# Optimization experiments

Hardware: AMD Instinct MI355X
Metric: run time of the kernel (lower is better)

Reference implementation:

```python
import jax, jax.numpy as jnp
import numpy as np

N = 100000   # nodes
E = 1000000  # edges (before self-loops)
F = 64       # feat_dim
H = 64       # hidden_dim
G = 512      # graphs in batch
EPS = 1e-5   # BatchNorm1d eps


def setup_inputs() -> dict:
    key = jax.random.key(0)
    ks = jax.random.split(key, 16)
    inp = {}
    inp["x"] = jax.random.normal(ks[0], (N, F), dtype=jnp.float32)
    inp["edge_index"] = jax.random.randint(ks[1], (2, E), 0, N)
    inp["batch"] = jnp.sort(jax.random.randint(ks[2], (N,), 0, G))
    dims = [(F, H), (H, H), (H, H)]
    for i, (di, do) in enumerate(dims):
        # xavier_uniform-scale weights, zero bias (as in weights_init)
        bound = np.sqrt(6.0 / (di + do)).astype(np.float32)
        inp[f"W{i}"] = jax.random.uniform(ks[3 + i], (do, di), dtype=jnp.float32,
                                          minval=-bound, maxval=bound)
        inp[f"b{i}"] = jnp.zeros((do,), dtype=jnp.float32)
        inp[f"g{i}"] = jnp.ones((do,), dtype=jnp.float32)
        inp[f"beta{i}"] = jnp.zeros((do,), dtype=jnp.float32)
    return inp


def reference(x, edge_index, batch,
              W0, b0, g0, beta0,
              W1, b1, g1, beta1,
              W2, b2, g2, beta2):
    # PyG GCNConv: add self-loops, norm = deg^-1/2[src] * deg^-1/2[dst]
    loops = jnp.arange(N)
    src = jnp.concatenate([edge_index[0], loops])  # source j
    dst = jnp.concatenate([edge_index[1], loops])  # target i
    deg = jax.ops.segment_sum(jnp.ones(src.shape, x.dtype), dst, num_segments=N)
    dinv = jnp.where(deg > 0, jax.lax.rsqrt(deg), 0.0)
    norm = dinv[src] * dinv[dst]  # [E+N]

    params = [(W0, b0, g0, beta0), (W1, b1, g1, beta1), (W2, b2, g2, beta2)]
    xs = []
    h = x
    for (W, b, g, beta) in params:
        h = h @ W.T                               # lin (no bias)
        msg = h[src] * norm[:, None]              # gather + scale  [E+N, H]
        h = jax.ops.segment_sum(msg, dst, num_segments=N) + b  # scatter-add + bias
        h = jax.nn.relu(h)
        # BatchNorm1d (training mode: biased batch stats)
        mean = h.mean(axis=0)
        var = h.var(axis=0)
        h = g * (h - mean) * jax.lax.rsqrt(var + EPS) + beta
        xs.append(h)

    # global_add_pool per layer output, then concat
    pooled = [jax.ops.segment_sum(xi, batch, num_segments=G) for xi in xs]
    global_rep = jnp.concatenate(pooled, axis=1)  # [G, 3*H]
    return global_rep, h
```

## Files before the change

### kernel.cpp

```cpp
#include <hip/hip_runtime.h>

#define HD 64
#define BN_EPS 1e-5f

typedef unsigned int u32;
typedef __attribute__((ext_vector_type(8))) short bfrag;
typedef __attribute__((ext_vector_type(4))) float ffrag;

__device__ __forceinline__ unsigned tobf(float x) {
    unsigned u = __float_as_uint(x);
    return (u + 0x7fffu + ((u >> 16) & 1u)) >> 16;
}
__device__ __forceinline__ float bf_lo(unsigned u) { return __uint_as_float(u << 16); }
__device__ __forceinline__ float bf_hi(unsigned u) { return __uint_as_float(u & 0xffff0000u); }


__global__ void k_deg(const int* __restrict__ dst, int* __restrict__ deg,
                      int* __restrict__ rank, int E) {
    int e = blockIdx.x * blockDim.x + threadIdx.x;
    if (e < E) {
        int d = __builtin_nontemporal_load(&dst[e]);
        int r = atomicAdd(&deg[d], 1);
        __builtin_nontemporal_store(r, &rank[e]);
    }
}

__global__ void k_scan1(const int* __restrict__ deg, int* __restrict__ incl,
                        int* __restrict__ bsums, float* __restrict__ dinv,
                        unsigned* __restrict__ hWs, int N) {
    __shared__ int s[256];
    int tid = threadIdx.x;
    int i = blockIdx.x * 256 + tid;
    if (blockIdx.x == 0 && tid < 32) hWs[(size_t)N * 32 + tid] = 0u;
    int d = (i < N) ? deg[i] : 0;
    int pd = (i < N) ? ((d + 8) & ~7) : 0;
    s[tid] = pd;
    __syncthreads();
    for (int off = 1; off < 256; off <<= 1) {
        int t = (tid >= off) ? s[tid - off] : 0;
        __syncthreads();
        s[tid] += t;
        __syncthreads();
    }
    if (i < N) {
        incl[i] = s[tid];
        dinv[i] = rsqrtf((float)(d + 1));
    }
    if (tid == 255) bsums[blockIdx.x] = s[255];
}

__global__ void k_scan3(int* __restrict__ rowp, const int* __restrict__ deg,
                        const int* __restrict__ incl, const int* __restrict__ bsums,
                        int* __restrict__ ed, int N, int nb) {
    __shared__ float red[256];
    int tid = threadIdx.x;
    int b = blockIdx.x;
    float psum = 0.f;
    for (int t = tid; t < b; t += 256) psum += (float)bsums[t];
    red[tid] = psum;
    __syncthreads();
    for (int off = 128; off > 0; off >>= 1) {
        if (tid < off) red[tid] += red[tid + off];
        __syncthreads();
    }
    int bpre = (int)red[0];
    int i = b * 256 + tid;
    if (i < N) {
        int d = deg[i];
        int pd = (d + 8) & ~7;
        int rv = incl[i] - pd + bpre;
        rowp[i] = rv;
        ed[rv] = i;
        for (int k = d + 1; k < pd; k++) ed[rv + k] = N;
        if (i == N - 1) rowp[N] = rv + pd;
    }
}

#define FILL_SLAB 4096
__global__ void k_fill(const int* __restrict__ src, const int* __restrict__ dst,
                       const int* __restrict__ rank, const int* __restrict__ rowp,
                       int* __restrict__ ed, const int* __restrict__ batch,
                       int* __restrict__ cnt, int E, int N, int G) {
    int tid = threadIdx.x;
    int gid = blockIdx.x * 256 + tid;
    if (gid < G) {
        int g = gid;
        int lo = 0, hi = N;
        while (lo < hi) { int mid = (lo + hi) >> 1; if (batch[mid] < g) lo = mid + 1; else hi = mid; }
        int lo2 = lo, hi2 = N;
        while (lo2 < hi2) { int mid = (lo2 + hi2) >> 1; if (batch[mid] < g + 1) lo2 = mid + 1; else hi2 = mid; }
        cnt[g] = lo2 - lo;
    }
    int part = blockIdx.x & 7;
    int base = (blockIdx.x >> 3) * FILL_SLAB;
    int end = min(base + FILL_SLAB, E);
    for (int e = base + tid; e < end; e += 256) {
        int d = __builtin_nontemporal_load(&dst[e]);
        if (((d >> 12) & 7) == part) {
            int s = __builtin_nontemporal_load(&src[e]);
            int r = __builtin_nontemporal_load(&rank[e]);
            ed[rowp[d] + 1 + r] = s;
        }
    }
}

template<int FP32IN>
__global__ __launch_bounds__(256) void k_gemm2(const void* __restrict__ Aptr,
                                               const void* __restrict__ Wptr,
                                               const float* __restrict__ cb,
                                               const float* __restrict__ dinv,
                                               unsigned short* __restrict__ hWs,
                                               int N, int ntiles) {
    int lane = threadIdx.x & 63;
    int m = lane & 15, quad = lane >> 4;
    bfrag wf[4][2];
    if (FP32IN) {
        const float* W = (const float*)Wptr;
#pragma unroll
        for (int ft = 0; ft < 4; ft++)
#pragma unroll
            for (int kf = 0; kf < 2; kf++) {
                const float4* p4 = (const float4*)(W + (ft * 16 + m) * HD + kf * 32 + quad * 8);
                float4 x0 = p4[0], x1 = p4[1];
                union { unsigned u[4]; bfrag b; } r;
                r.u[0] = tobf(x0.x) | (tobf(x0.y) << 16);
                r.u[1] = tobf(x0.z) | (tobf(x0.w) << 16);
                r.u[2] = tobf(x1.x) | (tobf(x1.y) << 16);
                r.u[3] = tobf(x1.z) | (tobf(x1.w) << 16);
                wf[ft][kf] = r.b;
            }
    } else {
        const unsigned short* W = (const unsigned short*)Wptr;
#pragma unroll
        for (int ft = 0; ft < 4; ft++)
#pragma unroll
            for (int kf = 0; kf < 2; kf++)
                wf[ft][kf] = *(const bfrag*)(W + (ft * 16 + m) * HD + kf * 32 + quad * 8);
    }
    float cbv[4];
#pragma unroll
    for (int ft = 0; ft < 4; ft++) cbv[ft] = cb ? cb[ft * 16 + m] : 0.f;

    int wid = (blockIdx.x * blockDim.x + threadIdx.x) >> 6;
    int nw = (gridDim.x * blockDim.x) >> 6;
    for (int tile = wid; tile < ntiles; tile += nw) {
        int arow = min(tile * 16 + m, N - 1);
        bfrag a0, a1;
        if (FP32IN) {
            const float4* p4 = (const float4*)((const float*)Aptr + (size_t)arow * HD + quad * 8);
            float4 x0 = p4[0], x1 = p4[1], y0 = p4[8], y1 = p4[9];
            union { unsigned u[4]; bfrag b; } r0, r1;
            r0.u[0] = tobf(x0.x) | (tobf(x0.y) << 16);
            r0.u[1] = tobf(x0.z) | (tobf(x0.w) << 16);
            r0.u[2] = tobf(x1.x) | (tobf(x1.y) << 16);
            r0.u[3] = tobf(x1.z) | (tobf(x1.w) << 16);
            r1.u[0] = tobf(y0.x) | (tobf(y0.y) << 16);
            r1.u[1] = tobf(y0.z) | (tobf(y0.w) << 16);
            r1.u[2] = tobf(y1.x) | (tobf(y1.y) << 16);
            r1.u[3] = tobf(y1.z) | (tobf(y1.w) << 16);
            a0 = r0.b; a1 = r1.b;
        } else {
            const unsigned short* p = (const unsigned short*)Aptr + (size_t)arow * HD + quad * 8;
            a0 = *(const bfrag*)p;
            a1 = *(const bfrag*)(p + 32);
        }
        ffrag acc[4];
#pragma unroll
        for (int ft = 0; ft < 4; ft++) {
            acc[ft] = (ffrag){0.f, 0.f, 0.f, 0.f};
            acc[ft] = __builtin_amdgcn_mfma_f32_16x16x32_bf16(a0, wf[ft][0], acc[ft], 0, 0, 0);
            acc[ft] = __builtin_amdgcn_mfma_f32_16x16x32_bf16(a1, wf[ft][1], acc[ft], 0, 0, 0);
        }
        int r0n = tile * 16 + quad * 4;
        float dv[4];
#pragma unroll
        for (int r = 0; r < 4; r++) dv[r] = dinv[min(r0n + r, N - 1)];
#pragma unroll
        for (int ft = 0; ft < 4; ft++)
#pragma unroll
            for (int r = 0; r < 4; r++) {
                int nrow = r0n + r;
                if (nrow < N) {
                    float v = (acc[ft][r] + cbv[ft]) * dv[r];
                    hWs[(size_t)nrow * HD + ft * 16 + m] = (unsigned short)tobf(v);
                }
            }
    }
}

__global__ __launch_bounds__(256) void k_agg(const int* __restrict__ rowp,
                                             const int* __restrict__ ed,
                                             const float* __restrict__ dinv,
                                             const unsigned* __restrict__ hWs,
                                             const float* __restrict__ bias,
                                             const int* __restrict__ batch,
                                             void* __restrict__ outp, int outBf,
                                             float* __restrict__ stats,
                                             float* __restrict__ praw,
                                             int N, int chunk,
                                             const float* __restrict__ gam,
                                             const float* __restrict__ bet,
                                             float* __restrict__ ss,
                                             const float* __restrict__ Wnext,
                                             unsigned* __restrict__ Wfb,
                                             float* __restrict__ cf,
                                             float invN, int* __restrict__ ticket) {
    __shared__ u32 sbuf[4][2][1024];
    int tid = threadIdx.x;
    int lane = tid & 63;
    int hf = lane >> 5;
    int m = lane & 31;
    int lsel = lane >> 3;
    int fsel = lane & 7;
    int wv = tid >> 6;
    int wid = blockIdx.x * 4 + wv;
    int i0 = wid * chunk, i1 = min(i0 + chunk, N);
    const uint4* hW4 = (const uint4*)hWs;
    float b0 = bias[2 * m], b1 = bias[2 * m + 1];
    float bs0 = 0.f, bs1 = 0.f, bq0 = 0.f, bq1 = 0.f;
    int curb = -1;
    float p0 = 0.f, p1 = 0.f;
    if (i0 < N) {
        int idx = i0 + lane;
        int rowv = rowp[min(idx, N)];
        float dinvv = dinv[min(idx, N - 1)];
        int batchv = batch[min(idx, N - 1)];
        int s0g = __shfl(rowv, 0);
        int send = __shfl(rowv, i1 - i0);
        int i = i0, ln = 0;
        int rem = (__shfl(rowv, 1) - s0g) >> 3;
        float acc0 = 0.f, acc1 = 0.f;
        int nst = (send - s0g + 31) >> 5;
        int sb = s0g;
        int eidx;
        { int id = sb + m; eidx = (id < send) ? __builtin_nontemporal_load(&ed[id]) : N; }
#pragma unroll
        for (int j = 0; j < 4; j++) {
            int sj = __shfl(eidx, j * 8 + lsel);
            __builtin_amdgcn_global_load_lds(
                (const __attribute__((address_space(1))) u32*)(hW4 + (size_t)sj * 8 + fsel),
                (__attribute__((address_space(3))) u32*)(&sbuf[wv][0][j * 256]),
                16, 0, 0);
        }
        int eidxN = N;
        if (nst > 1) { int id = sb + 32 + m; eidxN = (id < send) ? __builtin_nontemporal_load(&ed[id]) : N; }
        for (int t = 0; t < nst; t++) {
            int cb = t & 1;
            asm volatile("s_waitcnt vmcnt(0)" ::: "memory");
            __builtin_amdgcn_sched_barrier(0);
            if (t + 1 < nst) {
#pragma unroll
                for (int j = 0; j < 4; j++) {
                    int sj = __shfl(eidxN, j * 8 + lsel);
                    __builtin_amdgcn_global_load_lds(
                        (const __attribute__((address_space(1))) u32*)(hW4 + (size_t)sj * 8 + fsel),
                        (__attribute__((address_space(3))) u32*)(&sbuf[wv][cb ^ 1][j * 256]),
                        16, 0, 0);
                }
                if (t + 2 < nst) { int id = sb + 64 + m; eidxN = (id < send) ? __builtin_nontemporal_load(&ed[id]) : N; }
            }
            const u32* cur = &sbuf[wv][cb][0];
            int ng = min(4, (send - sb) >> 3);
            for (int g = 0; g < ng; g++) {
                u32 u[4];
#pragma unroll
                for (int tt = 0; tt < 4; tt++)
                    u[tt] = cur[(g * 8 + hf + 2 * tt) * 32 + m];
#pragma unroll
                for (int tt = 0; tt < 4; tt++) { acc0 += bf_lo(u[tt]); acc1 += bf_hi(u[tt]); }
                if (--rem == 0) {
                    float s0 = acc0 + __shfl_xor(acc0, 32);
                    float s1 = acc1 + __shfl_xor(acc1, 32);
                    float di = __shfl(dinvv, ln);
                    int b = __shfl(batchv, ln);
                    float h0 = fmaxf(fmaf(di, s0, b0), 0.f);
                    float h1 = fmaxf(fmaf(di, s1, b1), 0.f);
                    if (lane < 32) {
                        if (outBf) ((unsigned*)outp)[(size_t)i * 32 + m] = tobf(h0) | (tobf(h1) << 16);
                        else ((float2*)outp)[(size_t)i * 32 + m] = make_float2(h0, h1);
                        bs0 += h0; bs1 += h1;
                        bq0 = fmaf(h0, h0, bq0); bq1 = fmaf(h1, h1, bq1);
                        if (b != curb) {
                            if (curb >= 0) {
                                atomicAdd(&praw[(size_t)curb * HD + 2 * m], p0);
                                atomicAdd(&praw[(size_t)curb * HD + 2 * m + 1], p1);
                            }
                            curb = b; p0 = h0; p1 = h1;
                        } else { p0 += h0; p1 += h1; }
                    }
                    i++; ln++;
                    rem = (i < i1) ? ((__shfl(rowv, ln + 1) - __shfl(rowv, ln)) >> 3)
                                   : 0x3fffffff;
                    acc0 = 0.f; acc1 = 0.f;
                }
            }
            sb += 32;
        }
    }
    if (lane < 32 && curb >= 0) {
        atomicAdd(&praw[(size_t)curb * HD + 2 * m], p0);
        atomicAdd(&praw[(size_t)curb * HD + 2 * m + 1], p1);
    }
    __shared__ float r1s[4][HD], r2s[4][HD];
    if (lane < 32) {
        r1s[wv][2 * m] = bs0; r1s[wv][2 * m + 1] = bs1;
        r2s[wv][2 * m] = bq0; r2s[wv][2 * m + 1] = bq1;
    }
    __syncthreads();
    if (tid < HD) {
        atomicAdd(&stats[tid], r1s[0][tid] + r1s[1][tid] + r1s[2][tid] + r1s[3][tid]);
        atomicAdd(&stats[HD + tid], r2s[0][tid] + r2s[1][tid] + r2s[2][tid] + r2s[3][tid]);
    }
    __shared__ int lastFlag;
    __syncthreads();
    if (tid == 0) {
        __threadfence();
        lastFlag = (atomicAdd(ticket, 1) == (int)gridDim.x - 1) ? 1 : 0;
    }
    __syncthreads();
    if (lastFlag) {
        __shared__ float lss[128];
        __shared__ float cpart[HD][4];
        if (tid < HD) {
            float s1v = atomicAdd(&stats[tid], 0.f);
            float s2v = atomicAdd(&stats[HD + tid], 0.f);
            float mean = s1v * invN;
            float var = s2v * invN - mean * mean;
            float sc = gam[tid] * rsqrtf(var + BN_EPS);
            float sh = bet[tid] - mean * sc;
            ss[tid] = sc; ss[64 + tid] = sh;
            lss[tid] = sc; lss[64 + tid] = sh;
        }
        __syncthreads();
        if (Wnext) {
            int r = tid >> 2, qs = (tid & 3) * 8;
            const float4* W4 = (const float4*)(Wnext + r * HD + 2 * qs);
            float c = 0.f;
#pragma unroll
            for (int t = 0; t < 4; t++) {
                float4 w = W4[t];
                int q = qs + 2 * t;
                Wfb[r * 32 + q]     = tobf(w.x * lss[2 * q])     | (tobf(w.y * lss[2 * q + 1]) << 16);
                Wfb[r * 32 + q + 1] = tobf(w.z * lss[2 * q + 2]) | (tobf(w.w * lss[2 * q + 3]) << 16);
                c = fmaf(lss[64 + 2 * q], w.x, c);
                c = fmaf(lss[64 + 2 * q + 1], w.y, c);
                c = fmaf(lss[64 + 2 * q + 2], w.z, c);
                c = fmaf(lss[64 + 2 * q + 3], w.w, c);
            }
            cpart[r][tid & 3] = c;
            __syncthreads();
            if (tid < HD)
                cf[tid] = cpart[tid][0] + cpart[tid][1] + cpart[tid][2] + cpart[tid][3];
        }
    }
}

__global__ __launch_bounds__(256) void k_fin(float* __restrict__ h,
                                             const float* __restrict__ ss_all,
                                             const float* __restrict__ praw,
                                             const int* __restrict__ cnt,
                                             float* __restrict__ pool,
                                             int nquads, int G) {
    int nb1 = (nquads + 255) >> 8;
    if ((int)blockIdx.x < nb1) {
        int idx = blockIdx.x * 256 + threadIdx.x;
        if (idx >= nquads) return;
        const float* ss = ss_all + 2 * 128;
        float4* h4 = (float4*)h;
        float4 v = h4[idx];
        int f0 = (idx * 4) & 63;
        v.x = fmaf(v.x, ss[f0 + 0], ss[64 + f0 + 0]);
        v.y = fmaf(v.y, ss[f0 + 1], ss[64 + f0 + 1]);
        v.z = fmaf(v.z, ss[f0 + 2], ss[64 + f0 + 2]);
        v.w = fmaf(v.w, ss[f0 + 3], ss[64 + f0 + 3]);
        h4[idx] = v;
    } else {
        int idx = (blockIdx.x - nb1) * 256 + threadIdx.x;
        if (idx >= G * 192) return;
        int g = idx / 192;
        int r = idx - g * 192;
        int l = r >> 6;
        int f = r & 63;
        const float* ss = ss_all + l * 128;
        float v = praw[((size_t)l * G + g) * HD + f];
        pool[idx] = fmaf(ss[f], v, (float)cnt[g] * ss[64 + f]);
    }
}

extern "C" void kernel_launch(void* const* d_in, const int* in_sizes, int n_in,
                              void* d_out, int out_size, void* d_ws, size_t ws_size,
                              hipStream_t stream) {
    const int N = in_sizes[0] / HD;
    const int E = in_sizes[1] / 2;
    const int G = (out_size - N * HD) / 192;

    const float* x = (const float*)d_in[0];
    const int* ei = (const int*)d_in[1];
    const int* srcA = ei;
    const int* dstA = ei + E;
    const int* batch = (const int*)d_in[2];
    const float* W[3]    = {(const float*)d_in[3], (const float*)d_in[7],  (const float*)d_in[11]};
    const float* bias[3] = {(const float*)d_in[4], (const float*)d_in[8],  (const float*)d_in[12]};
    const float* gam[3]  = {(const float*)d_in[5], (const float*)d_in[9],  (const float*)d_in[13]};
    const float* bet[3]  = {(const float*)d_in[6], (const float*)d_in[10], (const float*)d_in[14]};

    char* ws = (char*)d_ws;
    size_t off = 0;
    auto alloc = [&](size_t bytes) -> void* {
        void* p = ws + off;
        off = (off + bytes + 255) & ~(size_t)255;
        return p;
    };
    int* deg     = (int*)alloc((size_t)N * 4);
    float* stats = (float*)alloc(3 * 128 * 4);
    int* tickets = (int*)alloc(3 * 4);
    float* praw  = (float*)alloc((size_t)3 * G * HD * 4);
    size_t zbytes = off;
    int* rank    = (int*)alloc((size_t)E * 4);
    float* dinv  = (float*)alloc((size_t)N * 4);
    int* rowp    = (int*)alloc((size_t)(N + 1) * 4);
    int* incl    = (int*)alloc((size_t)N * 4);
    int* bsums   = (int*)alloc(512 * 4);
    int* ed      = (int*)alloc(((size_t)E + 8 * (size_t)N) * 4 + 512);
    unsigned short* hWs  = (unsigned short*)alloc((size_t)(N + 1) * HD * 2);
    unsigned short* hraw = (unsigned short*)alloc((size_t)N * HD * 2);
    float* ss    = (float*)alloc(3 * 128 * 4);
    unsigned* Wfb = (unsigned*)alloc(2 * HD * 32 * 4);
    float* cf    = (float*)alloc(2 * HD * 4);
    int* gcnt    = (int*)alloc((size_t)G * 4);
    (void)ws_size;

    float* pool = (float*)d_out;
    float* hbuf = (float*)d_out + (size_t)G * 192;

    hipMemsetAsync(deg, 0, zbytes, stream);

    int nb = (N + 255) / 256;
    k_deg<<<(E + 255) / 256, 256, 0, stream>>>(dstA, deg, rank, E);
    k_scan1<<<nb, 256, 0, stream>>>(deg, incl, bsums, dinv, (unsigned*)hWs, N);
    k_scan3<<<nb, 256, 0, stream>>>(rowp, deg, incl, bsums, ed, N, nb);
    int nslab = (E + FILL_SLAB - 1) / FILL_SLAB;
    k_fill<<<nslab * 8, 256, 0, stream>>>(srcA, dstA, rank, rowp, ed, batch, gcnt, E, N, G);

    const int AGG_BLOCKS = 1024;
    const int NW = AGG_BLOCKS * 4;
    const int chunk = (N + NW - 1) / NW;
    const int ntiles = (N + 15) / 16;

    for (int l = 0; l < 3; l++) {
        if (l == 0)
            k_gemm2<1><<<640, 256, 0, stream>>>(x, W[0], nullptr, dinv, hWs, N, ntiles);
        else
            k_gemm2<0><<<640, 256, 0, stream>>>(hraw, Wfb + (size_t)(l - 1) * HD * 32,
                                                cf + (l - 1) * HD, dinv, hWs, N, ntiles);
        void* outp = (l < 2) ? (void*)hraw : (void*)hbuf;
        k_agg<<<AGG_BLOCKS, 256, 0, stream>>>(rowp, ed, dinv, (const unsigned*)hWs,
                                              bias[l], batch, outp, (l < 2) ? 1 : 0,
                                              stats + l * 128, praw + (size_t)l * G * HD,
                                              N, chunk,
                                              gam[l], bet[l], ss + l * 128,
                                              (l < 2) ? W[l + 1] : nullptr,
                                              Wfb + (size_t)(l < 2 ? l : 0) * HD * 32,
                                              cf + (l < 2 ? l : 0) * HD,
                                              1.0f / (float)N, tickets + l);
    }
    int nquads = N * HD / 4;
    int nb1 = (nquads + 255) / 256;
    int nb2 = (G * 192 + 255) / 256;
    k_fin<<<nb1 + nb2, 256, 0, stream>>>(hbuf, ss, praw, gcnt, pool, nquads, G);
}
```

Baseline: 416.9 us.

## Split aggregation into four feature-slice passes over a sliced hW layout

Stores the transformed features hWs and hraw as four 16-feature slices of 32 bytes per node instead of one 128-byte row. Aggregation now runs as four launches per layer, one per slice, so each gather touches a smaller and more cache-friendly working set, with a wave-wide shuffle reduction and a doubled block count. The degree pass also drops the per-edge rank array and uses partitioned atomics plus a cursor atomic in the fill kernel. In exchange the edge list is re-read four times per layer and the ticket-based last-block finalization now spans four launches.

```diff
diff --git a/kernel.cpp b/kernel.cpp
--- a/kernel.cpp
+++ b/kernel.cpp
@@ -4,6 +4,7 @@
 #define BN_EPS 1e-5f
 
 typedef unsigned int u32;
+typedef unsigned long long u64;
 typedef __attribute__((ext_vector_type(8))) short bfrag;
 typedef __attribute__((ext_vector_type(4))) float ffrag;
 
@@ -15,13 +16,16 @@
 __device__ __forceinline__ float bf_hi(unsigned u) { return __uint_as_float(u & 0xffff0000u); }
 
 
-__global__ void k_deg(const int* __restrict__ dst, int* __restrict__ deg,
-                      int* __restrict__ rank, int E) {
-    int e = blockIdx.x * blockDim.x + threadIdx.x;
-    if (e < E) {
+#define FILL_SLAB 4096
+
+__global__ void k_deg(const int* __restrict__ dst, int* __restrict__ deg, int E) {
+    int tid = threadIdx.x;
+    int part = blockIdx.x & 7;
+    int base = (blockIdx.x >> 3) * FILL_SLAB;
+    int end = min(base + FILL_SLAB, E);
+    for (int e = base + tid; e < end; e += 256) {
         int d = __builtin_nontemporal_load(&dst[e]);
-        int r = atomicAdd(&deg[d], 1);
-        __builtin_nontemporal_store(r, &rank[e]);
+        if (((d >> 12) & 7) == part) atomicAdd(&deg[d], 1);
     }
 }
 
@@ -31,7 +35,9 @@
     __shared__ int s[256];
     int tid = threadIdx.x;
     int i = blockIdx.x * 256 + tid;
-    if (blockIdx.x == 0 && tid < 32) hWs[(size_t)N * 32 + tid] = 0u;
+    if (blockIdx.x == 0 && tid < 32) {
+        hWs[(size_t)(tid >> 3) * (N + 1) * 8 + (size_t)N * 8 + (tid & 7)] = 0u;
+    }
     int d = (i < N) ? deg[i] : 0;
     int pd = (i < N) ? ((d + 8) & ~7) : 0;
     s[tid] = pd;
@@ -76,9 +82,8 @@
     }
 }
 
-#define FILL_SLAB 4096
 __global__ void k_fill(const int* __restrict__ src, const int* __restrict__ dst,
-                       const int* __restrict__ rank, const int* __restrict__ rowp,
+                       const int* __restrict__ rowp, int* __restrict__ cur,
                        int* __restrict__ ed, const int* __restrict__ batch,
                        int* __restrict__ cnt, int E, int N, int G) {
     int tid = threadIdx.x;
@@ -98,8 +103,8 @@
         int d = __builtin_nontemporal_load(&dst[e]);
         if (((d >> 12) & 7) == part) {
             int s = __builtin_nontemporal_load(&src[e]);
-            int r = __builtin_nontemporal_load(&rank[e]);
-            ed[rowp[d] + 1 + r] = s;
+            int pos = rowp[d] + 1 + atomicAdd(&cur[d], 1);
+            ed[pos] = s;
         }
     }
 }
@@ -160,9 +165,9 @@
             r1.u[3] = tobf(y1.z) | (tobf(y1.w) << 16);
             a0 = r0.b; a1 = r1.b;
         } else {
-            const unsigned short* p = (const unsigned short*)Aptr + (size_t)arow * HD + quad * 8;
-            a0 = *(const bfrag*)p;
-            a1 = *(const bfrag*)(p + 32);
+            const unsigned short* A = (const unsigned short*)Aptr;
+            a0 = *(const bfrag*)(A + ((size_t)(quad >> 1) * N + arow) * 16 + (quad & 1) * 8);
+            a1 = *(const bfrag*)(A + ((size_t)((quad >> 1) + 2) * N + arow) * 16 + (quad & 1) * 8);
         }
         ffrag acc[4];
 #pragma unroll
@@ -182,41 +187,40 @@
                 int nrow = r0n + r;
                 if (nrow < N) {
                     float v = (acc[ft][r] + cbv[ft]) * dv[r];
-                    hWs[(size_t)nrow * HD + ft * 16 + m] = (unsigned short)tobf(v);
+                    hWs[((size_t)ft * (N + 1) + nrow) * 16 + m] = (unsigned short)tobf(v);
                 }
             }
     }
 }
 
-__global__ __launch_bounds__(256) void k_agg(const int* __restrict__ rowp,
-                                             const int* __restrict__ ed,
-                                             const float* __restrict__ dinv,
-                                             const unsigned* __restrict__ hWs,
-                                             const float* __restrict__ bias,
-                                             const int* __restrict__ batch,
-                                             void* __restrict__ outp, int outBf,
-                                             float* __restrict__ stats,
-                                             float* __restrict__ praw,
-                                             int N, int chunk,
-                                             const float* __restrict__ gam,
-                                             const float* __restrict__ bet,
-                                             float* __restrict__ ss,
-                                             const float* __restrict__ Wnext,
-                                             unsigned* __restrict__ Wfb,
-                                             float* __restrict__ cf,
-                                             float invN, int* __restrict__ ticket) {
-    __shared__ u32 sbuf[4][2][1024];
+__global__ __launch_bounds__(256) void k_aggs(const int* __restrict__ rowp,
+                                              const int* __restrict__ ed,
+                                              const float* __restrict__ dinv,
+                                              const unsigned* __restrict__ hWs,
+                                              const float* __restrict__ bias,
+                                              const int* __restrict__ batch,
+                                              void* __restrict__ outp, int outBf,
+                                              float* __restrict__ stats,
+                                              float* __restrict__ praw,
+                                              int N, int chunk, int slice,
+                                              const float* __restrict__ gam,
+                                              const float* __restrict__ bet,
+                                              float* __restrict__ ss,
+                                              const float* __restrict__ Wnext,
+                                              unsigned* __restrict__ Wfb,
+                                              float* __restrict__ cf,
+                                              float invN, int* __restrict__ ticket,
+                                              int nticket) {
+    __shared__ u32 sbuf[4][2][512];
     int tid = threadIdx.x;
     int lane = tid & 63;
-    int hf = lane >> 5;
-    int m = lane & 31;
-    int lsel = lane >> 3;
-    int fsel = lane & 7;
+    int ls = lane >> 3;
+    int fp = lane & 7;
     int wv = tid >> 6;
     int wid = blockIdx.x * 4 + wv;
     int i0 = wid * chunk, i1 = min(i0 + chunk, N);
-    const uint4* hW4 = (const uint4*)hWs;
-    float b0 = bias[2 * m], b1 = bias[2 * m + 1];
+    const uint4* hW4 = (const uint4*)hWs + (size_t)slice * (N + 1) * 2;
+    float b0 = bias[slice * 16 + 2 * fp], b1 = bias[slice * 16 + 2 * fp + 1];
     float bs0 = 0.f, bs1 = 0.f, bq0 = 0.f, bq1 = 0.f;
     int curb = -1;
     float p0 = 0.f, p1 = 0.f;
@@ -230,60 +234,65 @@
         int i = i0, ln = 0;
         int rem = (__shfl(rowv, 1) - s0g) >> 3;
         float acc0 = 0.f, acc1 = 0.f;
-        int nst = (send - s0g + 31) >> 5;
+        int nst = (send - s0g + 63) >> 6;
         int sb = s0g;
         int eidx;
-        { int id = sb + m; eidx = (id < send) ? __builtin_nontemporal_load(&ed[id]) : N; }
-#pragma unroll
-        for (int j = 0; j < 4; j++) {
-            int sj = __shfl(eidx, j * 8 + lsel);
+        { int id = sb + lane; eidx = (id < send) ? __builtin_nontemporal_load(&ed[id]) : N; }
+#pragma unroll
+        for (int j = 0; j < 2; j++) {
+            int sj = __shfl(eidx, j * 32 + (lane >> 1));
             __builtin_amdgcn_global_load_lds(
-                (const __attribute__((address_space(1))) u32*)(hW4 + (size_t)sj * 8 + fsel),
+                (const __attribute__((address_space(1))) u32*)(hW4 + (size_t)sj * 2 + (lane & 1)),
                 (__attribute__((address_space(3))) u32*)(&sbuf[wv][0][j * 256]),
                 16, 0, 0);
         }
         int eidxN = N;
-        if (nst > 1) { int id = sb + 32 + m; eidxN = (id < send) ? __builtin_nontemporal_load(&ed[id]) : N; }
+        if (nst > 1) { int id = sb + 64 + lane; eidxN = (id < send) ? __builtin_nontemporal_load(&ed[id]) : N; }
         for (int t = 0; t < nst; t++) {
             int cb = t & 1;
             asm volatile("s_waitcnt vmcnt(0)" ::: "memory");
             __builtin_amdgcn_sched_barrier(0);
             if (t + 1 < nst) {
 #pragma unroll
-                for (int j = 0; j < 4; j++) {
-                    int sj = __shfl(eidxN, j * 8 + lsel);
+                for (int j = 0; j < 2; j++) {
+                    int sj = __shfl(eidxN, j * 32 + (lane >> 1));
                     __builtin_amdgcn_global_load_lds(
-                        (const __attribute__((address_space(1))) u32*)(hW4 + (size_t)sj * 8 + fsel),
+                        (const __attribute__((address_space(1))) u32*)(hW4 + (size_t)sj * 2 + (lane & 1)),
                         (__attribute__((address_space(3))) u32*)(&sbuf[wv][cb ^ 1][j * 256]),
                         16, 0, 0);
                 }
-                if (t + 2 < nst) { int id = sb + 64 + m; eidxN = (id < send) ? __builtin_nontemporal_load(&ed[id]) : N; }
+                if (t + 2 < nst) { int id = sb + 128 + lane; eidxN = (id < send) ? __builtin_nontemporal_load(&ed[id]) : N; }
             }
             const u32* cur = &sbuf[wv][cb][0];
-            int ng = min(4, (send - sb) >> 3);
+            int ng = min(8, (send - sb) >> 3);
             for (int g = 0; g < ng; g++) {
-                u32 u[4];
-#pragma unroll
-                for (int tt = 0; tt < 4; tt++)
-                    u[tt] = cur[(g * 8 + hf + 2 * tt) * 32 + m];
-#pragma unroll
-                for (int tt = 0; tt < 4; tt++) { acc0 += bf_lo(u[tt]); acc1 += bf_hi(u[tt]); }
+                u32 u = cur[g * 64 + ls * 8 + fp];
+                float f0 = bf_lo(u), f1 = bf_hi(u);
+                f0 += __shfl_xor(f0, 8);  f1 += __shfl_xor(f1, 8);
+                f0 += __shfl_xor(f0, 16); f1 += __shfl_xor(f1, 16);
+                f0 += __shfl_xor(f0, 32); f1 += __shfl_xor(f1, 32);
+                acc0 += f0; acc1 += f1;
                 if (--rem == 0) {
-                    float s0 = acc0 + __shfl_xor(acc0, 32);
-                    float s1 = acc1 + __shfl_xor(acc1, 32);
                     float di = __shfl(dinvv, ln);
                     int b = __shfl(batchv, ln);
-                    float h0 = fmaxf(fmaf(di, s0, b0), 0.f);
-                    float h1 = fmaxf(fmaf(di, s1, b1), 0.f);
-                    if (lane < 32) {
-                        if (outBf) ((unsigned*)outp)[(size_t)i * 32 + m] = tobf(h0) | (tobf(h1) << 16);
-                        else ((float2*)outp)[(size_t)i * 32 + m] = make_float2(h0, h1);
+                    float h0 = fmaxf(fmaf(di, acc0, b0), 0.f);
+                    float h1 = fmaxf(fmaf(di, acc1, b1), 0.f);
+                    if (lane < 8) {
+                        if (outBf) {
+                            __builtin_nontemporal_store(tobf(h0) | (tobf(h1) << 16),
+                                &((unsigned*)outp)[((size_t)slice * N + i) * 8 + fp]);
+                        } else {
+                            union { float2 f; u64 v; } o;
+                            o.f = make_float2(h0, h1);
+                            __builtin_nontemporal_store(o.v,
+                                (u64*)&((float2*)outp)[(size_t)i * 32 + slice * 8 + fp]);
+                        }
                         bs0 += h0; bs1 += h1;
                         bq0 = fmaf(h0, h0, bq0); bq1 = fmaf(h1, h1, bq1);
                         if (b != curb) {
                             if (curb >= 0) {
-                                atomicAdd(&praw[(size_t)curb * HD + 2 * m], p0);
-                                atomicAdd(&praw[(size_t)curb * HD + 2 * m + 1], p1);
+                                atomicAdd(&praw[(size_t)curb * HD + slice * 16 + 2 * fp], p0);
+                                atomicAdd(&praw[(size_t)curb * HD + slice * 16 + 2 * fp + 1], p1);
                             }
                             curb = b; p0 = h0; p1 = h1;
                         } else { p0 += h0; p1 += h1; }
@@ -294,28 +303,28 @@
                     acc0 = 0.f; acc1 = 0.f;
                 }
             }
-            sb += 32;
-        }
-    }
-    if (lane < 32 && curb >= 0) {
-        atomicAdd(&praw[(size_t)curb * HD + 2 * m], p0);
-        atomicAdd(&praw[(size_t)curb * HD + 2 * m + 1], p1);
-    }
-    __shared__ float r1s[4][HD], r2s[4][HD];
-    if (lane < 32) {
-        r1s[wv][2 * m] = bs0; r1s[wv][2 * m + 1] = bs1;
-        r2s[wv][2 * m] = bq0; r2s[wv][2 * m + 1] = bq1;
+            sb += 64;
+        }
+    }
+    if (lane < 8 && curb >= 0) {
+        atomicAdd(&praw[(size_t)curb * HD + slice * 16 + 2 * fp], p0);
+        atomicAdd(&praw[(size_t)curb * HD + slice * 16 + 2 * fp + 1], p1);
+    }
+    __shared__ float r1s[4][16], r2s[4][16];
+    if (lane < 8) {
+        r1s[wv][2 * fp] = bs0; r1s[wv][2 * fp + 1] = bs1;
+        r2s[wv][2 * fp] = bq0; r2s[wv][2 * fp + 1] = bq1;
     }
     __syncthreads();
-    if (tid < HD) {
-        atomicAdd(&stats[tid], r1s[0][tid] + r1s[1][tid] + r1s[2][tid] + r1s[3][tid]);
-        atomicAdd(&stats[HD + tid], r2s[0][tid] + r2s[1][tid] + r2s[2][tid] + r2s[3][tid]);
+    if (tid < 16) {
+        atomicAdd(&stats[slice * 16 + tid], r1s[0][tid] + r1s[1][tid] + r1s[2][tid] + r1s[3][tid]);
+        atomicAdd(&stats[64 + slice * 16 + tid], r2s[0][tid] + r2s[1][tid] + r2s[2][tid] + r2s[3][tid]);
     }
     __shared__ int lastFlag;
     __syncthreads();
     if (tid == 0) {
         __threadfence();
-        lastFlag = (atomicAdd(ticket, 1) == (int)gridDim.x - 1) ? 1 : 0;
+        lastFlag = (atomicAdd(ticket, 1) == nticket - 1) ? 1 : 0;
     }
     __syncthreads();
     if (lastFlag) {
@@ -412,18 +421,18 @@
         return p;
     };
     int* deg     = (int*)alloc((size_t)N * 4);
+    int* cur     = (int*)alloc((size_t)N * 4);
     float* stats = (float*)alloc(3 * 128 * 4);
     int* tickets = (int*)alloc(3 * 4);
     float* praw  = (float*)alloc((size_t)3 * G * HD * 4);
     size_t zbytes = off;
-    int* rank    = (int*)alloc((size_t)E * 4);
     float* dinv  = (float*)alloc((size_t)N * 4);
     int* rowp    = (int*)alloc((size_t)(N + 1) * 4);
     int* incl    = (int*)alloc((size_t)N * 4);
     int* bsums   = (int*)alloc(512 * 4);
     int* ed      = (int*)alloc(((size_t)E + 8 * (size_t)N) * 4 + 512);
-    unsigned short* hWs  = (unsigned short*)alloc((size_t)(N + 1) * HD * 2);
-    unsigned short* hraw = (unsigned short*)alloc((size_t)N * HD * 2);
+    unsigned short* hWs  = (unsigned short*)alloc((size_t)4 * (N + 1) * 16 * 2);
+    unsigned short* hraw = (unsigned short*)alloc((size_t)4 * N * 16 * 2);
     float* ss    = (float*)alloc(3 * 128 * 4);
     unsigned* Wfb = (unsigned*)alloc(2 * HD * 32 * 4);
     float* cf    = (float*)alloc(2 * HD * 4);
@@ -436,13 +445,13 @@
     hipMemsetAsync(deg, 0, zbytes, stream);
 
     int nb = (N + 255) / 256;
-    k_deg<<<(E + 255) / 256, 256, 0, stream>>>(dstA, deg, rank, E);
+    int nslab = (E + FILL_SLAB - 1) / FILL_SLAB;
+    k_deg<<<nslab * 8, 256, 0, stream>>>(dstA, deg, E);
     k_scan1<<<nb, 256, 0, stream>>>(deg, incl, bsums, dinv, (unsigned*)hWs, N);
     k_scan3<<<nb, 256, 0, stream>>>(rowp, deg, incl, bsums, ed, N, nb);
-    int nslab = (E + FILL_SLAB - 1) / FILL_SLAB;
-    k_fill<<<nslab * 8, 256, 0, stream>>>(srcA, dstA, rank, rowp, ed, batch, gcnt, E, N, G);
-
-    const int AGG_BLOCKS = 1024;
+    k_fill<<<nslab * 8, 256, 0, stream>>>(srcA, dstA, rowp, cur, ed, batch, gcnt, E, N, G);
+
+    const int AGG_BLOCKS = 2048;
     const int NW = AGG_BLOCKS * 4;
     const int chunk = (N + NW - 1) / NW;
     const int ntiles = (N + 15) / 16;
@@ -454,15 +463,18 @@
             k_gemm2<0><<<640, 256, 0, stream>>>(hraw, Wfb + (size_t)(l - 1) * HD * 32,
                                                 cf + (l - 1) * HD, dinv, hWs, N, ntiles);
         void* outp = (l < 2) ? (void*)hraw : (void*)hbuf;
-        k_agg<<<AGG_BLOCKS, 256, 0, stream>>>(rowp, ed, dinv, (const unsigned*)hWs,
-                                              bias[l], batch, outp, (l < 2) ? 1 : 0,
-                                              stats + l * 128, praw + (size_t)l * G * HD,
-                                              N, chunk,
-                                              gam[l], bet[l], ss + l * 128,
-                                              (l < 2) ? W[l + 1] : nullptr,
-                                              Wfb + (size_t)(l < 2 ? l : 0) * HD * 32,
-                                              cf + (l < 2 ? l : 0) * HD,
-                                              1.0f / (float)N, tickets + l);
+        for (int s = 0; s < 4; s++) {
+            k_aggs<<<AGG_BLOCKS, 256, 0, stream>>>(rowp, ed, dinv, (const unsigned*)hWs,
+                                                   bias[l], batch, outp, (l < 2) ? 1 : 0,
+                                                   stats + l * 128, praw + (size_t)l * G * HD,
+                                                   N, chunk, s,
+                                                   gam[l], bet[l], ss + l * 128,
+                                                   (l < 2) ? W[l + 1] : nullptr,
+                                                   Wfb + (size_t)(l < 2 ? l : 0) * HD * 32,
+                                                   cf + (l < 2 ? l : 0) * HD,
+                                                   1.0f / (float)N, tickets + l,
+                                                   4 * AGG_BLOCKS);
+        }
     }
     int nquads = N * HD / 4;
     int nb1 = (nquads + 255) / 256;
```

Result: slower. 1.120 ms (+168.6%).
